# Kernel tuning notes

Hardware: AMD Instinct MI355X
Metric: run time of the kernel (lower is better)

The kernel has to match this reference:

```python
import jax, jax.numpy as jnp
import numpy as np

B, H, V = 64, 512, 20000
Lc, Lce, Lkb, R, E, T = 128, 64, 256, 32, 128, 32
SOS = 2
NEG = -1e9


def setup_inputs() -> dict:
    key = jax.random.key(0)
    ks = jax.random.split(key, 24)
    f = lambda i, shape, s: (jax.random.normal(ks[i], shape) * s).astype(jnp.float32)
    return dict(
        context_hidden=f(0, (1, B, H), 1.0),
        context_outputs=f(1, (B, Lc, H), 1.0),
        context_entity=f(2, (B, Lce, H), 1.0),
        kb_entity=f(3, (B, Lkb, H), 1.0),
        embed=f(4, (V, H), 0.1),
        Wp=f(5, (H, H), 0.05), bp=jnp.zeros((H,), jnp.float32),
        Wih=f(6, (3 * H, H), 0.05), Whh=f(7, (3 * H, H), 0.05),
        bih=jnp.zeros((3 * H,), jnp.float32), bhh=jnp.zeros((3 * H,), jnp.float32),
        Wg_ce=f(8, (H, H), 0.05), Wg_kb=f(9, (H, H), 0.05),
        Wq=f(10, (H, H), 0.05), Wm=f(11, (H, H), 0.05),
        v_attn=f(12, (H,), 0.05), b_attn=jnp.zeros((H,), jnp.float32),
        Wsw=f(13, (1, H), 0.05), bsw=jnp.zeros((1,), jnp.float32),
        Wc=f(14, (H, 3 * H), 0.05), bc=jnp.zeros((H,), jnp.float32),
        Wv=f(15, (V, H), 0.05), bv=jnp.zeros((V,), jnp.float32),
        context_entity_id=jax.random.randint(ks[16], (B, Lce), 0, E),
        kb_entity_id=jax.random.randint(ks[17], (B, Lkb), 0, E),
        kb_entity_row=jax.random.randint(ks[18], (B, Lkb), 0, R),
        context_mask=jnp.zeros((B, Lc), bool),
        context_entity_mask=jnp.zeros((B, Lce), bool),
        kb_entity_mask=jnp.zeros((B, Lkb), bool),
        target=jax.random.randint(ks[19], (B, T), 0, V),
    )


def gru_cell(x, h, Wih, Whh, bih, bhh):
    gi = x @ Wih.T + bih
    gh = h @ Whh.T + bhh
    ir, iz, inn = jnp.split(gi, 3, axis=-1)
    hr, hz, hn = jnp.split(gh, 3, axis=-1)
    r = jax.nn.sigmoid(ir + hr)
    z = jax.nn.sigmoid(iz + hz)
    n = jnp.tanh(inn + r * hn)
    return (1.0 - z) * n + z * h


def reference(context_hidden, context_outputs, context_entity, kb_entity,
              embed, Wp, bp, Wih, Whh, bih, bhh, Wg_ce, Wg_kb, Wq, Wm,
              v_attn, b_attn, Wsw, bsw, Wc, bc, Wv, bv,
              context_entity_id, kb_entity_id, kb_entity_row,
              context_mask, context_entity_mask, kb_entity_mask, target):
    B_, T_ = target.shape
    rows = jnp.arange(B_)[:, None]
    # dec_hidden = relu(projector(context_hidden))
    h0 = jax.nn.relu(context_hidden[0] @ Wp.T + bp)  # [B,H]
    # teacher forcing: input at step t is SOS for t=0, else target[:, t-1]
    dec_inputs = jnp.concatenate(
        [jnp.full((B_, 1), SOS, target.dtype), target[:, :-1]], axis=1)  # [B,T]

    # time-invariant KB row aggregation (to_onehot + bmm)
    onehot = jax.nn.one_hot(kb_entity_row, R, dtype=jnp.float32)
    onehot = onehot * (~kb_entity_mask)[..., None].astype(jnp.float32)  # [B,Lkb,R]
    row_onehot = jnp.swapaxes(onehot, 1, 2)  # [B,R,Lkb]
    row_hidden = jnp.einsum('brk,bkh->brh', row_onehot, kb_entity)  # [B,R,H]
    row_cnt = row_onehot.sum(2, keepdims=True)  # [B,R,1]
    row_empty = row_cnt[..., 0] == 0  # [B,R]
    row_hidden = row_hidden / jnp.clip(row_cnt, 1.0, None)
    # time-invariant mlp-attention memory projection
    mem_proj = jnp.einsum('bkh,gh->bkg', context_outputs, Wm)  # [B,Lc,H]

    def step(h, inp_t):
        x = embed[inp_t]  # [B,H] (dropout=0.0)
        h = gru_cell(x, h, Wih, Whh, bih, bhh)
        q = h
        # context-entity attention (general)
        qe = q @ Wg_ce.T
        logit_ce = jnp.einsum('bh,bkh->bk', qe, context_entity)
        logit_ce = jnp.where(context_entity_mask, NEG, logit_ce)
        w_ce = jax.nn.softmax(logit_ce, axis=1)
        ce_hidden = jnp.einsum('bk,bkh->bh', w_ce, context_entity)
        p_ctx = jnp.zeros((B_, E), jnp.float32).at[rows, context_entity_id].add(w_ce)
        # kb row-level attention (general)
        qk = q @ Wg_kb.T
        logit_row = jnp.einsum('bh,brh->br', qk, row_hidden)
        logit_row = jnp.where(row_empty, NEG, logit_row)
        w_row = jax.nn.softmax(logit_row, axis=1)
        kb_hidden = jnp.einsum('br,brh->bh', w_row, row_hidden)
        kb_row_pro = jnp.einsum('br,brk->bk', w_row, row_onehot)  # [B,Lkb]
        # within-row kb distribution: broadcast logits masked by row one-hot
        logit_kb = jnp.einsum('bh,bkh->bk', qk, kb_entity)[:, None, :]  # [B,1,Lkb]
        logit_kb = jnp.where(row_onehot > 0, logit_kb, NEG)  # [B,R,Lkb]
        pro_in_row = jax.nn.softmax(logit_kb, axis=2)
        pro_pos = jnp.take_along_axis(pro_in_row, kb_entity_row[:, None, :], axis=1)[:, 0, :]
        kb_pro = pro_pos * kb_row_pro  # [B,Lkb]
        p_kb = jnp.zeros((B_, E), jnp.float32).at[rows, kb_entity_id].add(kb_pro)
        # switch gate
        psw = jax.nn.sigmoid(q @ Wsw.T + bsw)  # [B,1]
        p_entity = (1.0 - psw) * p_ctx + psw * p_kb
        # mlp attention over context outputs
        logit_c = jnp.einsum('h,bkh->bk', v_attn,
                             jnp.tanh((q @ Wq.T)[:, None, :] + mem_proj + b_attn))
        logit_c = jnp.where(context_mask, NEG, logit_c)
        w_c = jax.nn.softmax(logit_c, axis=1)
        vocab_attn = jnp.einsum('bk,bkh->bh', w_c, context_outputs)
        entity_hidden = ce_hidden * (1.0 - psw) + kb_hidden * psw
        concat_out = jnp.tanh(
            jnp.concatenate([q, vocab_attn, entity_hidden], axis=1) @ Wc.T + bc)
        p_vocab = concat_out @ Wv.T + bv
        return h, (p_vocab, p_entity)

    _, (vocab_out, ptr_out) = jax.lax.scan(step, h0, dec_inputs.T)
    return vocab_out, ptr_out  # [T,B,V], [T,B,E]
```

## Files before the change

kernel.cpp:

```cpp
#include <hip/hip_runtime.h>
#include <math.h>


#define BN   64
#define HN   512
#define VN   20000
#define LCN  128
#define LCEN 64
#define LKBN 256
#define RN   32
#define EN   128
#define TN   32
#define NEGV -1e9f

typedef __attribute__((ext_vector_type(8))) short bf16x8;
typedef __attribute__((ext_vector_type(4))) float f32x4;

__device__ __forceinline__ float fast_tanh(float x) {
  float ax = fabsf(x);
  float e = __expf(-2.f * ax);
  float r = __fdividef(1.f - e, 1.f + e);
  return copysignf(r, x);
}
__device__ __forceinline__ float fast_sigm(float x) {
  return __fdividef(1.f, 1.f + __expf(-x));
}

__device__ __forceinline__ unsigned short f2bf(float f) {
  unsigned int u = __float_as_uint(f);
  unsigned int r = (u + 0x7FFFu + ((u >> 16) & 1u)) >> 16;
  return (unsigned short)r;
}

__device__ __forceinline__ void split8(const float* v, bf16x8& hi, bf16x8& lo) {
#pragma unroll
  for (int i = 0; i < 8; ++i) {
    unsigned short h = f2bf(v[i]);
    hi[i] = (short)h;
    lo[i] = (short)f2bf(v[i] - __uint_as_float((unsigned int)h << 16));
  }
}

template <int ACT, int TRS>
__global__ __launch_bounds__(256) void gemm_tile64(
    const float* __restrict__ A, const float* __restrict__ W,
    const float* __restrict__ bias, float* __restrict__ C,
    int M, int N, int K)
{
  __shared__ float As[16][68];
  __shared__ float Ws[16][68];
  int tid = threadIdx.x;
  int m0 = blockIdx.x * 64, n0 = blockIdx.y * 64;
  int lr = tid >> 2;
  int lk = (tid & 3) << 2;
  int ty = tid >> 4, tx = tid & 15;
  float acc[4][4] = {};
  const float* Ap = A + (size_t)(m0 + lr) * K + lk;
  const float* Wp = W + (size_t)(n0 + lr) * K + lk;
  bool aok = (m0 + lr) < M;
  bool wok = (n0 + lr) < N;
  for (int k0 = 0; k0 < K; k0 += 16) {
    float4 av = aok ? *(const float4*)(Ap + k0) : make_float4(0.f, 0.f, 0.f, 0.f);
    float4 wv = wok ? *(const float4*)(Wp + k0) : make_float4(0.f, 0.f, 0.f, 0.f);
    As[lk + 0][lr] = av.x; As[lk + 1][lr] = av.y; As[lk + 2][lr] = av.z; As[lk + 3][lr] = av.w;
    Ws[lk + 0][lr] = wv.x; Ws[lk + 1][lr] = wv.y; Ws[lk + 2][lr] = wv.z; Ws[lk + 3][lr] = wv.w;
    __syncthreads();
#pragma unroll
    for (int kk = 0; kk < 16; ++kk) {
      float4 a = *(const float4*)&As[kk][ty << 2];
      float4 w = *(const float4*)&Ws[kk][tx << 2];
      float ar[4] = {a.x, a.y, a.z, a.w};
      float wr[4] = {w.x, w.y, w.z, w.w};
#pragma unroll
      for (int i = 0; i < 4; ++i)
#pragma unroll
        for (int j = 0; j < 4; ++j) acc[i][j] += ar[i] * wr[j];
    }
    __syncthreads();
  }
#pragma unroll
  for (int i = 0; i < 4; ++i) {
    int m = m0 + (ty << 2) + i;
    if (m >= M) continue;
#pragma unroll
    for (int j = 0; j < 4; ++j) {
      int n = n0 + (tx << 2) + j;
      if (n >= N) continue;
      float v = acc[i][j] + (bias ? bias[n] : 0.f);
      if (ACT == 1) v = fmaxf(v, 0.f);
      if (TRS)
        C[((size_t)(m >> 7) * N + n) * 128 + (m & 127)] = v;
      else
        C[(size_t)m * N + n] = v;
    }
  }
}

template <int EPI, bool GATHER, bool PROJ>
__global__ __launch_bounds__(256) void gemm_mfma(
    const float* __restrict__ A, const float* __restrict__ W, int wstride,
    const float* __restrict__ bias, const int* __restrict__ target,
    const float* __restrict__ addm, int astride,
    const float* __restrict__ Wce, const float* __restrict__ Wkb,
    const float* __restrict__ Wq, const float* __restrict__ Wc,
    float* __restrict__ Cf, unsigned short* __restrict__ Cb,
    int M, int N, int K)
{
  int tid = threadIdx.x, wv = tid >> 6, lane = tid & 63;
  int m0 = blockIdx.x * 64, n0 = blockIdx.y * 64;
  int wm = (wv >> 1) * 32, wn = (wv & 1) * 32;
  int lr = lane & 15, kg = (lane >> 4) * 8;

  const float* arow[2];
#pragma unroll
  for (int mt = 0; mt < 2; ++mt) {
    int m = m0 + wm + mt * 16 + lr;
    if (GATHER) {
      int tt = m >> 6, bb = m & 63;
      int tok = (tt == 0) ? 2 : target[bb * TN + (tt - 1)];
      arow[mt] = A + (size_t)tok * K + kg;
    } else {
      arow[mt] = A + (size_t)m * K + kg;
    }
  }
  const float* wrow[2];
#pragma unroll
  for (int nt = 0; nt < 2; ++nt) {
    int nr = n0 + wn + nt * 16 + lr;
    if (PROJ) {
      if (nr < 512)       wrow[nt] = Wce + (size_t)nr * 512 + kg;
      else if (nr < 1024) wrow[nt] = Wkb + (size_t)(nr - 512) * 512 + kg;
      else if (nr < 1536) wrow[nt] = Wq + (size_t)(nr - 1024) * 512 + kg;
      else                wrow[nt] = Wc + (size_t)(nr - 1536) * 1536 + kg;
    } else {
      wrow[nt] = W + (size_t)nr * wstride + kg;
    }
  }

  f32x4 acc[2][2];
#pragma unroll
  for (int i = 0; i < 2; ++i)
#pragma unroll
    for (int j = 0; j < 2; ++j) acc[i][j] = (f32x4){0.f, 0.f, 0.f, 0.f};

  for (int ko = 0; ko < K; ko += 32) {
    bf16x8 ah[2], al[2], bh[2], bl[2];
#pragma unroll
    for (int mt = 0; mt < 2; ++mt) {
      float av[8];
      *(float4*)(av + 0) = *(const float4*)(arow[mt] + ko);
      *(float4*)(av + 4) = *(const float4*)(arow[mt] + ko + 4);
      split8(av, ah[mt], al[mt]);
    }
#pragma unroll
    for (int nt = 0; nt < 2; ++nt) {
      float wv8[8];
      *(float4*)(wv8 + 0) = *(const float4*)(wrow[nt] + ko);
      *(float4*)(wv8 + 4) = *(const float4*)(wrow[nt] + ko + 4);
      split8(wv8, bh[nt], bl[nt]);
    }
#pragma unroll
    for (int mt = 0; mt < 2; ++mt)
#pragma unroll
      for (int nt = 0; nt < 2; ++nt) {
        acc[mt][nt] = __builtin_amdgcn_mfma_f32_16x16x32_bf16(ah[mt], bh[nt], acc[mt][nt], 0, 0, 0);
        acc[mt][nt] = __builtin_amdgcn_mfma_f32_16x16x32_bf16(ah[mt], bl[nt], acc[mt][nt], 0, 0, 0);
        acc[mt][nt] = __builtin_amdgcn_mfma_f32_16x16x32_bf16(al[mt], bh[nt], acc[mt][nt], 0, 0, 0);
      }
  }

#pragma unroll
  for (int mt = 0; mt < 2; ++mt)
#pragma unroll
    for (int nt = 0; nt < 2; ++nt) {
      int col = n0 + wn + nt * 16 + lr;
      int rowb = m0 + wm + mt * 16 + (lane >> 4) * 4;
#pragma unroll
      for (int r = 0; r < 4; ++r) {
        int m = rowb + r;
        float v = acc[mt][nt][r];
        if (EPI == 0) {
          if (bias) v += bias[col];
          Cf[(size_t)m * N + col] = v;
        } else if (EPI == 2) {
          v += addm[(size_t)m * astride + col] + bias[col];
          Cb[(size_t)m * N + col] = f2bf(fast_tanh(v));
        } else {
          Cf[((size_t)(m >> 7) * N + col) * 128 + (m & 127)] = v;
        }
      }
    }
}

__global__ __launch_bounds__(256) void conv_bf16(
    const float* __restrict__ in, unsigned short* __restrict__ out, int n)
{
  int i = (blockIdx.x * 256 + threadIdx.x) * 4;
  if (i >= n) return;
  float4 v = *(const float4*)(in + i);
  out[i + 0] = f2bf(v.x);
  out[i + 1] = f2bf(v.y);
  out[i + 2] = f2bf(v.z);
  out[i + 3] = f2bf(v.w);
}

__global__ __launch_bounds__(256) void split_bf16k(
    const float* __restrict__ in, unsigned short* __restrict__ hi,
    unsigned short* __restrict__ lo, int n)
{
  int i = (blockIdx.x * 256 + threadIdx.x) * 4;
  if (i >= n) return;
  float4 v = *(const float4*)(in + i);
  float vv[4] = {v.x, v.y, v.z, v.w};
#pragma unroll
  for (int j = 0; j < 4; ++j) {
    unsigned short h = f2bf(vv[j]);
    hi[i + j] = h;
    lo[i + j] = f2bf(vv[j] - __uint_as_float((unsigned int)h << 16));
  }
}

__global__ __launch_bounds__(256) void row_agg(
    const float* __restrict__ kb, const int* __restrict__ krow,
    float* __restrict__ rowh, float* __restrict__ rowc)
{
  int b = blockIdx.x, tid = threadIdx.x;
  __shared__ float acc[RN * 256];
  __shared__ int rows[256];
  __shared__ float cnt_s[RN];
  rows[tid] = krow[b * LKBN + tid];
  __syncthreads();
  if (tid < RN) {
    int c = 0;
    for (int k = 0; k < LKBN; ++k) c += (rows[k] == tid);
    cnt_s[tid] = (float)c;
    rowc[b * RN + tid] = (float)c;
  }
  __syncthreads();
  for (int half = 0; half < 2; ++half) {
    int h = (half << 8) + tid;
    for (int r = 0; r < RN; ++r) acc[r * 256 + tid] = 0.f;
    for (int k = 0; k < LKBN; ++k)
      acc[rows[k] * 256 + tid] += kb[((size_t)b * LKBN + k) * HN + h];
    for (int r = 0; r < RN; ++r)
      rowh[((size_t)b * RN + r) * HN + h] = acc[r * 256 + tid] / fmaxf(cnt_s[r], 1.f);
  }
}

__global__ __launch_bounds__(256) void build_csr(
    const int* __restrict__ kbid, const int* __restrict__ ceid,
    const int* __restrict__ krow,
    int* __restrict__ kbo, int* __restrict__ kbi,
    int* __restrict__ ceo, int* __restrict__ cei,
    int* __restrict__ rwo, int* __restrict__ rwi)
{
  int b = blockIdx.x, tid = threadIdx.x;
  __shared__ int sid[256], srw[256], scid[64];
  __shared__ int cnt[128], off[129];
  sid[tid] = kbid[b * LKBN + tid];
  srw[tid] = krow[b * LKBN + tid];
  if (tid < 64) scid[tid] = ceid[b * LCEN + tid];
  __syncthreads();
  if (tid < 128) {
    int c = 0;
    for (int k = 0; k < 256; ++k) c += (sid[k] == tid);
    cnt[tid] = c;
  }
  __syncthreads();
  if (tid == 0) {
    int o = 0;
    for (int e = 0; e < 128; ++e) { off[e] = o; o += cnt[e]; }
    off[128] = o;
  }
  __syncthreads();
  if (tid < 128) {
    int w = off[tid];
    for (int k = 0; k < 256; ++k) if (sid[k] == tid) kbi[b * 256 + (w++)] = k;
    kbo[b * 129 + tid] = off[tid];
    if (tid == 0) kbo[b * 129 + 128] = off[128];
  }
  __syncthreads();
  if (tid < 128) {
    int c = 0;
    for (int k = 0; k < 64; ++k) c += (scid[k] == tid);
    cnt[tid] = c;
  }
  __syncthreads();
  if (tid == 0) {
    int o = 0;
    for (int e = 0; e < 128; ++e) { off[e] = o; o += cnt[e]; }
    off[128] = o;
  }
  __syncthreads();
  if (tid < 128) {
    int w = off[tid];
    for (int k = 0; k < 64; ++k) if (scid[k] == tid) cei[b * 64 + (w++)] = k;
    ceo[b * 129 + tid] = off[tid];
    if (tid == 0) ceo[b * 129 + 128] = off[128];
  }
  __syncthreads();
  if (tid < 32) {
    int c = 0;
    for (int k = 0; k < 256; ++k) c += (srw[k] == tid);
    cnt[tid] = c;
  }
  __syncthreads();
  if (tid == 0) {
    int o = 0;
    for (int r = 0; r < 32; ++r) { off[r] = o; o += cnt[r]; }
    off[32] = o;
  }
  __syncthreads();
  if (tid < 32) {
    int w = off[tid];
    for (int k = 0; k < 256; ++k) if (srw[k] == tid) rwi[b * 256 + (w++)] = k;
    rwo[b * 33 + tid] = off[tid];
    if (tid == 0) rwo[b * 33 + 32] = off[32];
  }
}

__global__ __launch_bounds__(256) void step_gru(
    const float* __restrict__ Gx, const float* __restrict__ hprev,
    float* __restrict__ hnew, const unsigned short* __restrict__ WhhH,
    const unsigned short* __restrict__ WhhL, const float* __restrict__ bhh)
{
  int tid = threadIdx.x;
  int wv = tid >> 6, lane = tid & 63;
  int j0 = blockIdx.x * 16;
  int m0 = wv * 16;
  int lr = lane & 15, kg = (lane >> 4) * 8;
  f32x4 acc[3];
#pragma unroll
  for (int g = 0; g < 3; ++g) acc[g] = (f32x4){0.f, 0.f, 0.f, 0.f};
  const float* ap = hprev + (size_t)(m0 + lr) * 512 + kg;
  const unsigned short* bhp = WhhH + (size_t)(j0 + lr) * 512 + kg;
  const unsigned short* blp = WhhL + (size_t)(j0 + lr) * 512 + kg;
#pragma unroll 4
  for (int ks = 0; ks < 16; ++ks) {
    int ko = ks * 32;
    float av[8];
    *(float4*)(av + 0) = *(const float4*)(ap + ko);
    *(float4*)(av + 4) = *(const float4*)(ap + ko + 4);
    bf16x8 ah, al;
    split8(av, ah, al);
#pragma unroll
    for (int g = 0; g < 3; ++g) {
      bf16x8 bh = *(const bf16x8*)(bhp + (size_t)g * 512 * 512 + ko);
      bf16x8 bl = *(const bf16x8*)(blp + (size_t)g * 512 * 512 + ko);
      acc[g] = __builtin_amdgcn_mfma_f32_16x16x32_bf16(ah, bh, acc[g], 0, 0, 0);
      acc[g] = __builtin_amdgcn_mfma_f32_16x16x32_bf16(ah, bl, acc[g], 0, 0, 0);
      acc[g] = __builtin_amdgcn_mfma_f32_16x16x32_bf16(al, bh, acc[g], 0, 0, 0);
    }
  }
  int j = j0 + lr;
#pragma unroll
  for (int r = 0; r < 4; ++r) {
    int b = m0 + (lane >> 4) * 4 + r;
    const float* gx = Gx + (size_t)b * 1536;
    float rr = fast_sigm(gx[j] + acc[0][r] + bhh[j]);
    float z  = fast_sigm(gx[512 + j] + acc[1][r] + bhh[512 + j]);
    float n  = fast_tanh(gx[1024 + j] + rr * (acc[2][r] + bhh[1024 + j]));
    float hp = hprev[(size_t)b * 512 + j];
    hnew[(size_t)b * 512 + j] = (1.f - z) * n + z * hp;
  }
}

__global__ __launch_bounds__(256) void attn_qk(
    const float* __restrict__ qp, const float* __restrict__ kb,
    const float* __restrict__ ce, const float* __restrict__ rowh,
    float* __restrict__ logits)
{
  int b = blockIdx.x, nt = blockIdx.y;
  int tid = threadIdx.x, wv = tid >> 6, lane = tid & 63;
  int lr = lane & 15, kg = (lane >> 4) * 8;
  const float* keys; int keybase, qoff, gkbase;
  if (nt < 8)       { keys = kb + (size_t)b * 256 * 512;  keybase = nt * 32;       qoff = 512; gkbase = keybase; }
  else if (nt < 10) { keys = ce + (size_t)b * 64 * 512;   keybase = (nt - 8) * 32; qoff = 0;   gkbase = 256 + keybase; }
  else              { keys = rowh + (size_t)b * 32 * 512; keybase = 0;             qoff = 512; gkbase = 320; }
  int mhalf = wv >> 1, nhalf = wv & 1;
  const float* ap = qp + (size_t)((mhalf * 16 + lr) * 64 + b) * 2048 + qoff + kg;
  const float* bp = keys + (size_t)(keybase + nhalf * 16 + lr) * 512 + kg;
  f32x4 acc = {0.f, 0.f, 0.f, 0.f};
#pragma unroll 4
  for (int ks = 0; ks < 16; ++ks) {
    int ko = ks * 32;
    float av[8], bv[8];
    *(float4*)(av + 0) = *(const float4*)(ap + ko);
    *(float4*)(av + 4) = *(const float4*)(ap + ko + 4);
    *(float4*)(bv + 0) = *(const float4*)(bp + ko);
    *(float4*)(bv + 4) = *(const float4*)(bp + ko + 4);
    bf16x8 ah, al, bh, bl;
    split8(av, ah, al);
    split8(bv, bh, bl);
    acc = __builtin_amdgcn_mfma_f32_16x16x32_bf16(ah, bh, acc, 0, 0, 0);
    acc = __builtin_amdgcn_mfma_f32_16x16x32_bf16(ah, bl, acc, 0, 0, 0);
    acc = __builtin_amdgcn_mfma_f32_16x16x32_bf16(al, bh, acc, 0, 0, 0);
  }
  int gk = gkbase + nhalf * 16 + lr;
#pragma unroll
  for (int r = 0; r < 4; ++r) {
    int t = mhalf * 16 + (lane >> 4) * 4 + r;
    logits[((size_t)b * 32 + t) * 352 + gk] = acc[r];
  }
}

__global__ __launch_bounds__(256) void attn_mlp(
    const float* __restrict__ qp, const float* __restrict__ mempT,
    const float* __restrict__ va, const float* __restrict__ ba,
    float* __restrict__ pmlp)
{
  int b = blockIdx.x, ch = blockIdx.y, tg = blockIdx.z;
  int tid = threadIdx.x;
  int h0 = ch << 7;
  __shared__ float sq[8][128];
  __shared__ float sv[128];
  for (int idx = tid; idx < 1024; idx += 256) {
    int tl = idx >> 7, i = idx & 127;
    int t = tg * 8 + tl;
    sq[tl][i] = qp[(size_t)(t * 64 + b) * 2048 + 1024 + h0 + i] + ba[h0 + i];
  }
  if (tid < 128) sv[tid] = va[h0 + tid];
  __syncthreads();
  int k = tid & 127, th = tid >> 7;
  const float* mp = mempT + ((size_t)b * 512 + h0) * 128 + k;
  float acc[4] = {};
  for (int h = 0; h < 128; ++h) {
    float mv = mp[h * 128];
    float vah = sv[h];
#pragma unroll
    for (int i = 0; i < 4; ++i)
      acc[i] += vah * fast_tanh(sq[th * 4 + i][h] + mv);
  }
#pragma unroll
  for (int i = 0; i < 4; ++i) {
    int t = tg * 8 + th * 4 + i;
    pmlp[(((size_t)b * 4 + ch) * 32 + t) * 128 + k] = acc[i];
  }
}

__global__ __launch_bounds__(256) void attn_reduce_all(
    const float* __restrict__ logits, const float* __restrict__ pmlp,
    const float* __restrict__ hall, const float* __restrict__ Wsw,
    const float* __restrict__ bsw, const int* __restrict__ krow,
    const int* __restrict__ kbo, const int* __restrict__ kbi,
    const int* __restrict__ ceo, const int* __restrict__ cei,
    const int* __restrict__ rwo, const int* __restrict__ rwi,
    float* __restrict__ pout, float* __restrict__ wall,
    float* __restrict__ pswall)
{
  int b = blockIdx.x, t = blockIdx.y, tid = threadIdx.x;
  int wv = tid >> 6, lane = tid & 63;
  __shared__ float s_l[480];
  __shared__ float s_kbp[256];
  __shared__ float s_wce[64], s_wrow[32], s_wc[128];
  __shared__ float s_rmax[32], s_rsum[32];
  __shared__ int s_krow[256];
  __shared__ float s_red[4];
  __shared__ float s_psw;

  const float* lg = logits + ((size_t)b * 32 + t) * 352;
  for (int k = tid; k < 352; k += 256) s_l[k] = lg[k];
  if (tid < 128) {
    const float* pm = pmlp + ((size_t)b * 4 * 32 + t) * 128 + tid;
    s_l[352 + tid] = pm[0] + pm[4096] + pm[8192] + pm[12288];
  }
  {
    const float* hp = hall + ((size_t)(t + 1) * 64 + b) * 512;
    float ps = hp[tid] * Wsw[tid] + hp[tid + 256] * Wsw[tid + 256];
    for (int o = 32; o; o >>= 1) ps += __shfl_down(ps, o);
    if (lane == 0) s_red[wv] = ps;
  }
  s_krow[tid] = krow[b * LKBN + tid];
  __syncthreads();
  if (tid == 0) s_psw = fast_sigm(s_red[0] + s_red[1] + s_red[2] + s_red[3] + bsw[0]);

  if (wv == 0) {
    {
      float v = s_l[256 + lane];
      float m = v;
      for (int o = 32; o; o >>= 1) m = fmaxf(m, __shfl_xor(m, o));
      float e = __expf(v - m), s = e;
      for (int o = 32; o; o >>= 1) s += __shfl_xor(s, o);
      s_wce[lane] = e / s;
    }
    {
      float v;
      if (lane < 32) {
        bool empty = rwo[b * 33 + lane + 1] == rwo[b * 33 + lane];
        v = empty ? NEGV : s_l[320 + lane];
      } else v = -INFINITY;
      float m = v;
      for (int o = 32; o; o >>= 1) m = fmaxf(m, __shfl_xor(m, o));
      float e = (lane < 32) ? __expf(v - m) : 0.f, s = e;
      for (int o = 32; o; o >>= 1) s += __shfl_xor(s, o);
      if (lane < 32) s_wrow[lane] = e / s;
    }
  } else if (wv == 1) {
    float v0 = s_l[352 + lane], v1 = s_l[352 + 64 + lane];
    float m = fmaxf(v0, v1);
    for (int o = 32; o; o >>= 1) m = fmaxf(m, __shfl_xor(m, o));
    float e0 = __expf(v0 - m), e1 = __expf(v1 - m);
    float s = e0 + e1;
    for (int o = 32; o; o >>= 1) s += __shfl_xor(s, o);
    s_wc[lane] = e0 / s;
    s_wc[lane + 64] = e1 / s;
  } else {
    int r = (tid - 128) >> 2, i = (tid - 128) & 3;
    int p0 = rwo[b * 33 + r], p1 = rwo[b * 33 + r + 1];
    float m = -INFINITY;
    for (int p = p0 + i; p < p1; p += 4) m = fmaxf(m, s_l[rwi[b * 256 + p]]);
    for (int o = 2; o; o >>= 1) m = fmaxf(m, __shfl_xor(m, o));
    float s = 0.f;
    for (int p = p0 + i; p < p1; p += 4) s += __expf(s_l[rwi[b * 256 + p]] - m);
    for (int o = 2; o; o >>= 1) s += __shfl_xor(s, o);
    if (i == 0) { s_rmax[r] = m; s_rsum[r] = s; }
  }
  __syncthreads();
  {
    int r = s_krow[tid];
    s_kbp[tid] = __expf(s_l[tid] - s_rmax[r]) / s_rsum[r] * s_wrow[r];
  }
  __syncthreads();
  if (tid < EN) {
    float a = 0.f;
    for (int p = ceo[b * 129 + tid]; p < ceo[b * 129 + tid + 1]; ++p)
      a += s_wce[cei[b * 64 + p]];
    float pk = 0.f;
    for (int p = kbo[b * 129 + tid]; p < kbo[b * 129 + tid + 1]; ++p)
      pk += s_kbp[kbi[b * 256 + p]];
    float psw = s_psw;
    pout[((size_t)t * BN + b) * EN + tid] = (1.f - psw) * a + psw * pk;
  }
  float* wb = wall + (size_t)(b * 32 + t) * 224;
  if (tid < 64) wb[tid] = s_wce[tid];
  else if (tid < 96) wb[tid] = s_wrow[tid - 64];
  else if (tid < 224) wb[tid] = s_wc[tid - 96];
  if (tid == 0) pswall[b * 32 + t] = s_psw;
}

__global__ __launch_bounds__(256) void attn_wsum_all(
    const float* __restrict__ wall, const float* __restrict__ pswall,
    const float* __restrict__ ctx, const float* __restrict__ ce,
    const float* __restrict__ rowh, float* __restrict__ cinall)
{
  int b = blockIdx.x, half = blockIdx.y, kind = blockIdx.z;
  int tid = threadIdx.x;
  int h = half * 256 + tid;
  if (kind == 0) {
    __shared__ float wc[32][128];
    for (int idx = tid; idx < 4096; idx += 256)
      wc[idx >> 7][idx & 127] = wall[(size_t)(b * 32 + (idx >> 7)) * 224 + 96 + (idx & 127)];
    __syncthreads();
    const float* xb = ctx + (size_t)b * 128 * 512 + h;
    float acc[32] = {};
    for (int k = 0; k < 128; k += 4) {
      float v0 = xb[(k + 0) * 512], v1 = xb[(k + 1) * 512];
      float v2 = xb[(k + 2) * 512], v3 = xb[(k + 3) * 512];
#pragma unroll
      for (int t = 0; t < 32; ++t) {
        float4 w = *(const float4*)&wc[t][k];
        acc[t] += w.x * v0 + w.y * v1 + w.z * v2 + w.w * v3;
      }
    }
    for (int t = 0; t < 32; ++t)
      cinall[(size_t)(t * 64 + b) * 1024 + h] = acc[t];
  } else {
    __shared__ float wce[32][64];
    __shared__ float wr[32][32];
    __shared__ float sps[32];
    for (int idx = tid; idx < 2048; idx += 256)
      wce[idx >> 6][idx & 63] = wall[(size_t)(b * 32 + (idx >> 6)) * 224 + (idx & 63)];
    for (int idx = tid; idx < 1024; idx += 256)
      wr[idx >> 5][idx & 31] = wall[(size_t)(b * 32 + (idx >> 5)) * 224 + 64 + (idx & 31)];
    if (tid < 32) sps[tid] = pswall[b * 32 + tid];
    __syncthreads();
    const float* cb = ce + (size_t)b * 64 * 512 + h;
    float ac[32] = {};
    for (int k = 0; k < 64; k += 4) {
      float v0 = cb[(k + 0) * 512], v1 = cb[(k + 1) * 512];
      float v2 = cb[(k + 2) * 512], v3 = cb[(k + 3) * 512];
#pragma unroll
      for (int t = 0; t < 32; ++t) {
        float4 w = *(const float4*)&wce[t][k];
        ac[t] += w.x * v0 + w.y * v1 + w.z * v2 + w.w * v3;
      }
    }
    const float* rb = rowh + (size_t)b * 32 * 512 + h;
    float ar[32] = {};
    for (int k = 0; k < 32; k += 4) {
      float v0 = rb[(k + 0) * 512], v1 = rb[(k + 1) * 512];
      float v2 = rb[(k + 2) * 512], v3 = rb[(k + 3) * 512];
#pragma unroll
      for (int t = 0; t < 32; ++t) {
        float4 w = *(const float4*)&wr[t][k];
        ar[t] += w.x * v0 + w.y * v1 + w.z * v2 + w.w * v3;
      }
    }
    for (int t = 0; t < 32; ++t) {
      float p = sps[t];
      cinall[(size_t)(t * 64 + b) * 1024 + 512 + h] = ac[t] * (1.f - p) + ar[t] * p;
    }
  }
}

__global__ __launch_bounds__(256) void gemm_vocab(
    const unsigned short* __restrict__ Ab, const unsigned short* __restrict__ Wb,
    const float* __restrict__ bv, float* __restrict__ C)
{
  int lid = blockIdx.x;
  int c = lid & 7, q = lid >> 3, i = q & 15, prow = q >> 4;
  int p = prow * 8 + c;
  if (p >= 157) return;
  int m0 = i * 128, n0 = p * 128;

  __shared__ __align__(16) unsigned short As[128 * 64];
  __shared__ __align__(16) unsigned short Bs[128 * 64];
  int tid = threadIdx.x;
  int wv = tid >> 6, lane = tid & 63;
  int wm = wv >> 1, wn = wv & 1;
  int srow = tid >> 3;
  int scb = (tid & 7) * 16;
  f32x4 acc[4][4];
#pragma unroll
  for (int a = 0; a < 4; ++a)
#pragma unroll
    for (int j = 0; j < 4; ++j) acc[a][j] = (f32x4){0.f, 0.f, 0.f, 0.f};

  for (int k0 = 0; k0 < 512; k0 += 64) {
    __syncthreads();
#pragma unroll
    for (int j = 0; j < 4; ++j) {
      int row = j * 32 + srow;
      uint4 va = *(const uint4*)(Ab + (size_t)(m0 + row) * 512 + k0 + (tid & 7) * 8);
      int brow = n0 + row;
      if (brow > VN - 1) brow = VN - 1;
      uint4 vb = *(const uint4*)(Wb + (size_t)brow * 512 + k0 + (tid & 7) * 8);
      int off = row * 128 + (scb ^ ((row & 7) << 4));
      *(uint4*)((char*)As + off) = va;
      *(uint4*)((char*)Bs + off) = vb;
    }
    __syncthreads();
#pragma unroll
    for (int ks = 0; ks < 2; ++ks) {
      bf16x8 af[4], bf[4];
#pragma unroll
      for (int m = 0; m < 4; ++m) {
        int r = wm * 64 + m * 16 + (lane & 15);
        int cb = (ks * 64 + (lane >> 4) * 16) ^ ((r & 7) << 4);
        af[m] = *(const bf16x8*)((const char*)As + r * 128 + cb);
      }
#pragma unroll
      for (int n = 0; n < 4; ++n) {
        int r = wn * 64 + n * 16 + (lane & 15);
        int cb = (ks * 64 + (lane >> 4) * 16) ^ ((r & 7) << 4);
        bf[n] = *(const bf16x8*)((const char*)Bs + r * 128 + cb);
      }
#pragma unroll
      for (int m = 0; m < 4; ++m)
#pragma unroll
        for (int n = 0; n < 4; ++n)
          acc[m][n] = __builtin_amdgcn_mfma_f32_16x16x32_bf16(af[m], bf[n], acc[m][n], 0, 0, 0);
    }
  }
#pragma unroll
  for (int n = 0; n < 4; ++n) {
    int col = n0 + wn * 64 + n * 16 + (lane & 15);
    if (col >= VN) continue;
    float bvv = bv[col];
#pragma unroll
    for (int m = 0; m < 4; ++m) {
      int rowb = m0 + wm * 64 + m * 16 + (lane >> 4) * 4;
#pragma unroll
      for (int r = 0; r < 4; ++r)
        C[(size_t)(rowb + r) * VN + col] = acc[m][n][r] + bvv;
    }
  }
}

extern "C" void kernel_launch(void* const* d_in, const int* in_sizes, int n_in,
                              void* d_out, int out_size, void* d_ws, size_t ws_size,
                              hipStream_t stream)
{
  const float* ch   = (const float*)d_in[0];
  const float* ctx  = (const float*)d_in[1];
  const float* ce   = (const float*)d_in[2];
  const float* kb   = (const float*)d_in[3];
  const float* emb  = (const float*)d_in[4];
  const float* Wp   = (const float*)d_in[5];
  const float* bp   = (const float*)d_in[6];
  const float* Wih  = (const float*)d_in[7];
  const float* Whh  = (const float*)d_in[8];
  const float* bih  = (const float*)d_in[9];
  const float* bhh  = (const float*)d_in[10];
  const float* Wgce = (const float*)d_in[11];
  const float* Wgkb = (const float*)d_in[12];
  const float* Wq   = (const float*)d_in[13];
  const float* Wm   = (const float*)d_in[14];
  const float* va   = (const float*)d_in[15];
  const float* ba   = (const float*)d_in[16];
  const float* Wsw  = (const float*)d_in[17];
  const float* bsw  = (const float*)d_in[18];
  const float* Wc   = (const float*)d_in[19];
  const float* bc   = (const float*)d_in[20];
  const float* Wv   = (const float*)d_in[21];
  const float* bv   = (const float*)d_in[22];
  const int* ce_id  = (const int*)d_in[23];
  const int* kb_id  = (const int*)d_in[24];
  const int* kb_row = (const int*)d_in[25];
  const int* target = (const int*)d_in[29];

  float* ws = (float*)d_ws;
  float* rowh   = ws;
  float* rowc   = rowh + 1048576;
  float* mempT  = rowc + 2048;
  float* hall   = mempT + 4194304;
  float* Gx     = hall + 1081344;
  float* qp     = Gx + 3145728;
  float* logits = qp + 4194304;
  float* pmlp   = logits + 720896;
  float* wall   = pmlp + 1048576;
  float* pswall = wall + 458752;
  float* cinall = pswall + 2048;
  unsigned short* callb = (unsigned short*)(cinall + 2097152);
  unsigned short* Wvb   = (unsigned short*)(cinall + 2097152 + 524288);
  unsigned short* WhhH  = (unsigned short*)(cinall + 2097152 + 524288 + 5120000);
  unsigned short* WhhL  = (unsigned short*)(cinall + 2097152 + 524288 + 5120000 + 393216);
  int* kbo = (int*)(cinall + 2097152 + 524288 + 5120000 + 786432);
  int* kbi = kbo + 64 * 129;
  int* ceo = kbi + 64 * 256;
  int* cei = ceo + 64 * 129;
  int* rwo = cei + 64 * 64;
  int* rwi = rwo + 64 * 33;

  float* vout = (float*)d_out;
  float* pout = vout + (size_t)TN * BN * VN;

  row_agg<<<BN, 256, 0, stream>>>(kb, kb_row, rowh, rowc);
  conv_bf16<<<10000, 256, 0, stream>>>(Wv, Wvb, VN * HN);
  split_bf16k<<<768, 256, 0, stream>>>(Whh, WhhH, WhhL, 1536 * 512);
  build_csr<<<BN, 256, 0, stream>>>(kb_id, ce_id, kb_row, kbo, kbi, ceo, cei,
                                    rwo, rwi);
  gemm_tile64<1, 0><<<dim3(1, 8), 256, 0, stream>>>(ch, Wp, bp, hall, BN, HN, HN);
  gemm_mfma<3, false, false><<<dim3(128, 8), 256, 0, stream>>>(
      ctx, Wm, 512, nullptr, nullptr, nullptr, 0,
      nullptr, nullptr, nullptr, nullptr, mempT, nullptr, 8192, 512, 512);
  gemm_mfma<0, true, false><<<dim3(32, 24), 256, 0, stream>>>(
      emb, Wih, 512, bih, target, nullptr, 0,
      nullptr, nullptr, nullptr, nullptr, Gx, nullptr, 2048, 1536, 512);

  for (int t = 0; t < TN; ++t)
    step_gru<<<32, 256, 0, stream>>>(
        Gx + (size_t)t * BN * 1536, hall + (size_t)t * BN * HN,
        hall + (size_t)(t + 1) * BN * HN, WhhH, WhhL, bhh);

  gemm_mfma<0, false, true><<<dim3(32, 32), 256, 0, stream>>>(
      hall + BN * HN, nullptr, 0, nullptr, nullptr, nullptr, 0,
      Wgce, Wgkb, Wq, Wc, qp, nullptr, 2048, 2048, 512);
  attn_qk<<<dim3(BN, 11), 256, 0, stream>>>(qp, kb, ce, rowh, logits);
  attn_mlp<<<dim3(BN, 4, 4), 256, 0, stream>>>(qp, mempT, va, ba, pmlp);
  attn_reduce_all<<<dim3(BN, TN), 256, 0, stream>>>(
      logits, pmlp, hall, Wsw, bsw, kb_row, kbo, kbi, ceo, cei, rwo, rwi,
      pout, wall, pswall);
  attn_wsum_all<<<dim3(BN, 2, 2), 256, 0, stream>>>(wall, pswall, ctx, ce,
                                                    rowh, cinall);
  gemm_mfma<2, false, false><<<dim3(32, 8), 256, 0, stream>>>(
      cinall, Wc + 512, 1536, bc, nullptr, qp + 1536, 2048,
      nullptr, nullptr, nullptr, nullptr, nullptr, callb, 2048, 512, 1024);
  gemm_vocab<<<2560, 256, 0, stream>>>(callb, Wvb, bv, vout);
}
```

Baseline: 1.168 ms.

## Persistent GRU kernel with grid barrier and merge setup/attention launches

Replaces the 32 per-timestep GRU launches with one persistent 32-block kernel that loops over timesteps and synchronises blocks through an atomic counter barrier in global memory. It also merges the two weight-conversion kernels, the row-aggregation and CSR-building kernels, and the two attention kernels into single launches to cut launch count. The spin barrier relies on all 32 blocks being co-resident. It adds a memset and fence/atomic latency per step.

```diff
diff --git a/kernel.cpp b/kernel.cpp
--- a/kernel.cpp
+++ b/kernel.cpp
@@ -192,44 +192,54 @@
     }
 }
 
-__global__ __launch_bounds__(256) void conv_bf16(
-    const float* __restrict__ in, unsigned short* __restrict__ out, int n)
-{
-  int i = (blockIdx.x * 256 + threadIdx.x) * 4;
-  if (i >= n) return;
-  float4 v = *(const float4*)(in + i);
-  out[i + 0] = f2bf(v.x);
-  out[i + 1] = f2bf(v.y);
-  out[i + 2] = f2bf(v.z);
-  out[i + 3] = f2bf(v.w);
-}
-
-__global__ __launch_bounds__(256) void split_bf16k(
-    const float* __restrict__ in, unsigned short* __restrict__ hi,
-    unsigned short* __restrict__ lo, int n)
-{
-  int i = (blockIdx.x * 256 + threadIdx.x) * 4;
-  if (i >= n) return;
-  float4 v = *(const float4*)(in + i);
-  float vv[4] = {v.x, v.y, v.z, v.w};
-#pragma unroll
-  for (int j = 0; j < 4; ++j) {
-    unsigned short h = f2bf(vv[j]);
-    hi[i + j] = h;
-    lo[i + j] = f2bf(vv[j] - __uint_as_float((unsigned int)h << 16));
-  }
-}
-
-__global__ __launch_bounds__(256) void row_agg(
+__global__ __launch_bounds__(256) void conv_split(
+    const float* __restrict__ Wv, unsigned short* __restrict__ Wvb,
+    const float* __restrict__ Whh, unsigned short* __restrict__ WhhH,
+    unsigned short* __restrict__ WhhL)
+{
+  int bid = blockIdx.x;
+  if (bid < 10000) {
+    int i = (bid * 256 + threadIdx.x) * 4;
+    if (i >= VN * HN) return;
+    float4 v = *(const float4*)(Wv + i);
+    Wvb[i + 0] = f2bf(v.x);
+    Wvb[i + 1] = f2bf(v.y);
+    Wvb[i + 2] = f2bf(v.z);
+    Wvb[i + 3] = f2bf(v.w);
+  } else {
+    int i = ((bid - 10000) * 256 + threadIdx.x) * 4;
+    if (i >= 1536 * 512) return;
+    float4 v = *(const float4*)(Whh + i);
+    float vv[4] = {v.x, v.y, v.z, v.w};
+#pragma unroll
+    for (int j = 0; j < 4; ++j) {
+      unsigned short h = f2bf(vv[j]);
+      WhhH[i + j] = h;
+      WhhL[i + j] = f2bf(vv[j] - __uint_as_float((unsigned int)h << 16));
+    }
+  }
+}
+
+__global__ __launch_bounds__(256) void setup_b(
     const float* __restrict__ kb, const int* __restrict__ krow,
-    float* __restrict__ rowh, float* __restrict__ rowc)
+    const int* __restrict__ kbid, const int* __restrict__ ceid,
+    float* __restrict__ rowh, float* __restrict__ rowc,
+    int* __restrict__ kbo, int* __restrict__ kbi,
+    int* __restrict__ ceo, int* __restrict__ cei,
+    int* __restrict__ rwo, int* __restrict__ rwi)
 {
   int b = blockIdx.x, tid = threadIdx.x;
   __shared__ float acc[RN * 256];
   __shared__ int rows[256];
   __shared__ float cnt_s[RN];
+  __shared__ int sid[256], scid[64];
+  __shared__ int cnt[128], off[129];
+
   rows[tid] = krow[b * LKBN + tid];
-  __syncthreads();
+  sid[tid] = kbid[b * LKBN + tid];
+  if (tid < 64) scid[tid] = ceid[b * LCEN + tid];
+  __syncthreads();
+
   if (tid < RN) {
     int c = 0;
     for (int k = 0; k < LKBN; ++k) c += (rows[k] == tid);
@@ -245,22 +255,8 @@
     for (int r = 0; r < RN; ++r)
       rowh[((size_t)b * RN + r) * HN + h] = acc[r * 256 + tid] / fmaxf(cnt_s[r], 1.f);
   }
-}
-
-__global__ __launch_bounds__(256) void build_csr(
-    const int* __restrict__ kbid, const int* __restrict__ ceid,
-    const int* __restrict__ krow,
-    int* __restrict__ kbo, int* __restrict__ kbi,
-    int* __restrict__ ceo, int* __restrict__ cei,
-    int* __restrict__ rwo, int* __restrict__ rwi)
-{
-  int b = blockIdx.x, tid = threadIdx.x;
-  __shared__ int sid[256], srw[256], scid[64];
-  __shared__ int cnt[128], off[129];
-  sid[tid] = kbid[b * LKBN + tid];
-  srw[tid] = krow[b * LKBN + tid];
-  if (tid < 64) scid[tid] = ceid[b * LCEN + tid];
-  __syncthreads();
+  __syncthreads();
+
   if (tid < 128) {
     int c = 0;
     for (int k = 0; k < 256; ++k) c += (sid[k] == tid);
@@ -301,7 +297,7 @@
   __syncthreads();
   if (tid < 32) {
     int c = 0;
-    for (int k = 0; k < 256; ++k) c += (srw[k] == tid);
+    for (int k = 0; k < 256; ++k) c += (rows[k] == tid);
     cnt[tid] = c;
   }
   __syncthreads();
@@ -313,128 +309,147 @@
   __syncthreads();
   if (tid < 32) {
     int w = off[tid];
-    for (int k = 0; k < 256; ++k) if (srw[k] == tid) rwi[b * 256 + (w++)] = k;
+    for (int k = 0; k < 256; ++k) if (rows[k] == tid) rwi[b * 256 + (w++)] = k;
     rwo[b * 33 + tid] = off[tid];
     if (tid == 0) rwo[b * 33 + 32] = off[32];
   }
 }
 
-__global__ __launch_bounds__(256) void step_gru(
-    const float* __restrict__ Gx, const float* __restrict__ hprev,
-    float* __restrict__ hnew, const unsigned short* __restrict__ WhhH,
-    const unsigned short* __restrict__ WhhL, const float* __restrict__ bhh)
+__global__ __launch_bounds__(256) void gru_chain(
+    const float* __restrict__ Gx0, float* __restrict__ hall,
+    const unsigned short* __restrict__ WhhH,
+    const unsigned short* __restrict__ WhhL,
+    const float* __restrict__ bhh, int* __restrict__ bar)
 {
   int tid = threadIdx.x;
   int wv = tid >> 6, lane = tid & 63;
   int j0 = blockIdx.x * 16;
   int m0 = wv * 16;
   int lr = lane & 15, kg = (lane >> 4) * 8;
-  f32x4 acc[3];
-#pragma unroll
-  for (int g = 0; g < 3; ++g) acc[g] = (f32x4){0.f, 0.f, 0.f, 0.f};
-  const float* ap = hprev + (size_t)(m0 + lr) * 512 + kg;
+  int j = j0 + lr;
   const unsigned short* bhp = WhhH + (size_t)(j0 + lr) * 512 + kg;
   const unsigned short* blp = WhhL + (size_t)(j0 + lr) * 512 + kg;
+
+  for (int t = 0; t < TN; ++t) {
+    const float* Gx = Gx0 + (size_t)t * BN * 1536;
+    const float* hprev = hall + (size_t)t * BN * HN;
+    float* hnew = hall + (size_t)(t + 1) * BN * HN;
+
+    f32x4 acc[3];
+#pragma unroll
+    for (int g = 0; g < 3; ++g) acc[g] = (f32x4){0.f, 0.f, 0.f, 0.f};
+    const float* ap = hprev + (size_t)(m0 + lr) * 512 + kg;
 #pragma unroll 4
-  for (int ks = 0; ks < 16; ++ks) {
-    int ko = ks * 32;
-    float av[8];
-    *(float4*)(av + 0) = *(const float4*)(ap + ko);
-    *(float4*)(av + 4) = *(const float4*)(ap + ko + 4);
-    bf16x8 ah, al;
-    split8(av, ah, al);
-#pragma unroll
-    for (int g = 0; g < 3; ++g) {
-      bf16x8 bh = *(const bf16x8*)(bhp + (size_t)g * 512 * 512 + ko);
-      bf16x8 bl = *(const bf16x8*)(blp + (size_t)g * 512 * 512 + ko);
-      acc[g] = __builtin_amdgcn_mfma_f32_16x16x32_bf16(ah, bh, acc[g], 0, 0, 0);
-      acc[g] = __builtin_amdgcn_mfma_f32_16x16x32_bf16(ah, bl, acc[g], 0, 0, 0);
-      acc[g] = __builtin_amdgcn_mfma_f32_16x16x32_bf16(al, bh, acc[g], 0, 0, 0);
-    }
-  }
-  int j = j0 + lr;
-#pragma unroll
-  for (int r = 0; r < 4; ++r) {
-    int b = m0 + (lane >> 4) * 4 + r;
-    const float* gx = Gx + (size_t)b * 1536;
-    float rr = fast_sigm(gx[j] + acc[0][r] + bhh[j]);
-    float z  = fast_sigm(gx[512 + j] + acc[1][r] + bhh[512 + j]);
-    float n  = fast_tanh(gx[1024 + j] + rr * (acc[2][r] + bhh[1024 + j]));
-    float hp = hprev[(size_t)b * 512 + j];
-    hnew[(size_t)b * 512 + j] = (1.f - z) * n + z * hp;
-  }
-}
-
-__global__ __launch_bounds__(256) void attn_qk(
+    for (int ks = 0; ks < 16; ++ks) {
+      int ko = ks * 32;
+      float av[8];
+      *(float4*)(av + 0) = *(const float4*)(ap + ko);
+      *(float4*)(av + 4) = *(const float4*)(ap + ko + 4);
+      bf16x8 ah, al;
+      split8(av, ah, al);
+#pragma unroll
+      for (int g = 0; g < 3; ++g) {
+        bf16x8 bh = *(const bf16x8*)(bhp + (size_t)g * 512 * 512 + ko);
+        bf16x8 bl = *(const bf16x8*)(blp + (size_t)g * 512 * 512 + ko);
+        acc[g] = __builtin_amdgcn_mfma_f32_16x16x32_bf16(ah, bh, acc[g], 0, 0, 0);
+        acc[g] = __builtin_amdgcn_mfma_f32_16x16x32_bf16(ah, bl, acc[g], 0, 0, 0);
+        acc[g] = __builtin_amdgcn_mfma_f32_16x16x32_bf16(al, bh, acc[g], 0, 0, 0);
+      }
+    }
+#pragma unroll
+    for (int r = 0; r < 4; ++r) {
+      int b = m0 + (lane >> 4) * 4 + r;
+      const float* gx = Gx + (size_t)b * 1536;
+      float rr = fast_sigm(gx[j] + acc[0][r] + bhh[j]);
+      float z  = fast_sigm(gx[512 + j] + acc[1][r] + bhh[512 + j]);
+      float n  = fast_tanh(gx[1024 + j] + rr * (acc[2][r] + bhh[1024 + j]));
+      float hp = hprev[(size_t)b * 512 + j];
+      hnew[(size_t)b * 512 + j] = (1.f - z) * n + z * hp;
+    }
+
+    if (t < TN - 1) {
+      __syncthreads();
+      if (tid == 0) {
+        __threadfence();
+        atomicAdd(bar, 1);
+        int target = 32 * (t + 1);
+        while (atomicAdd(bar, 0) < target) __builtin_amdgcn_s_sleep(2);
+      }
+      __syncthreads();
+      __threadfence();
+    }
+  }
+}
+
+__global__ __launch_bounds__(256) void attn_logits(
     const float* __restrict__ qp, const float* __restrict__ kb,
     const float* __restrict__ ce, const float* __restrict__ rowh,
-    float* __restrict__ logits)
+    const float* __restrict__ mempT, const float* __restrict__ va,
+    const float* __restrict__ ba, float* __restrict__ logits,
+    float* __restrict__ pmlp)
 {
   int b = blockIdx.x, nt = blockIdx.y;
-  int tid = threadIdx.x, wv = tid >> 6, lane = tid & 63;
-  int lr = lane & 15, kg = (lane >> 4) * 8;
-  const float* keys; int keybase, qoff, gkbase;
-  if (nt < 8)       { keys = kb + (size_t)b * 256 * 512;  keybase = nt * 32;       qoff = 512; gkbase = keybase; }
-  else if (nt < 10) { keys = ce + (size_t)b * 64 * 512;   keybase = (nt - 8) * 32; qoff = 0;   gkbase = 256 + keybase; }
-  else              { keys = rowh + (size_t)b * 32 * 512; keybase = 0;             qoff = 512; gkbase = 320; }
-  int mhalf = wv >> 1, nhalf = wv & 1;
-  const float* ap = qp + (size_t)((mhalf * 16 + lr) * 64 + b) * 2048 + qoff + kg;
-  const float* bp = keys + (size_t)(keybase + nhalf * 16 + lr) * 512 + kg;
-  f32x4 acc = {0.f, 0.f, 0.f, 0.f};
+  int tid = threadIdx.x;
+  if (nt < 11) {
+    int wv = tid >> 6, lane = tid & 63;
+    int lr = lane & 15, kg = (lane >> 4) * 8;
+    const float* keys; int keybase, qoff, gkbase;
+    if (nt < 8)       { keys = kb + (size_t)b * 256 * 512;  keybase = nt * 32;       qoff = 512; gkbase = keybase; }
+    else if (nt < 10) { keys = ce + (size_t)b * 64 * 512;   keybase = (nt - 8) * 32; qoff = 0;   gkbase = 256 + keybase; }
+    else              { keys = rowh + (size_t)b * 32 * 512; keybase = 0;             qoff = 512; gkbase = 320; }
+    int mhalf = wv >> 1, nhalf = wv & 1;
+    const float* ap = qp + (size_t)((mhalf * 16 + lr) * 64 + b) * 2048 + qoff + kg;
+    const float* bp = keys + (size_t)(keybase + nhalf * 16 + lr) * 512 + kg;
+    f32x4 acc = {0.f, 0.f, 0.f, 0.f};
 #pragma unroll 4
-  for (int ks = 0; ks < 16; ++ks) {
-    int ko = ks * 32;
-    float av[8], bv[8];
-    *(float4*)(av + 0) = *(const float4*)(ap + ko);
-    *(float4*)(av + 4) = *(const float4*)(ap + ko + 4);
-    *(float4*)(bv + 0) = *(const float4*)(bp + ko);
-    *(float4*)(bv + 4) = *(const float4*)(bp + ko + 4);
-    bf16x8 ah, al, bh, bl;
-    split8(av, ah, al);
-    split8(bv, bh, bl);
-    acc = __builtin_amdgcn_mfma_f32_16x16x32_bf16(ah, bh, acc, 0, 0, 0);
-    acc = __builtin_amdgcn_mfma_f32_16x16x32_bf16(ah, bl, acc, 0, 0, 0);
-    acc = __builtin_amdgcn_mfma_f32_16x16x32_bf16(al, bh, acc, 0, 0, 0);
-  }
-  int gk = gkbase + nhalf * 16 + lr;
-#pragma unroll
-  for (int r = 0; r < 4; ++r) {
-    int t = mhalf * 16 + (lane >> 4) * 4 + r;
-    logits[((size_t)b * 32 + t) * 352 + gk] = acc[r];
-  }
-}
-
-__global__ __launch_bounds__(256) void attn_mlp(
-    const float* __restrict__ qp, const float* __restrict__ mempT,
-    const float* __restrict__ va, const float* __restrict__ ba,
-    float* __restrict__ pmlp)
-{
-  int b = blockIdx.x, ch = blockIdx.y, tg = blockIdx.z;
-  int tid = threadIdx.x;
-  int h0 = ch << 7;
-  __shared__ float sq[8][128];
-  __shared__ float sv[128];
-  for (int idx = tid; idx < 1024; idx += 256) {
-    int tl = idx >> 7, i = idx & 127;
-    int t = tg * 8 + tl;
-    sq[tl][i] = qp[(size_t)(t * 64 + b) * 2048 + 1024 + h0 + i] + ba[h0 + i];
-  }
-  if (tid < 128) sv[tid] = va[h0 + tid];
-  __syncthreads();
-  int k = tid & 127, th = tid >> 7;
-  const float* mp = mempT + ((size_t)b * 512 + h0) * 128 + k;
-  float acc[4] = {};
-  for (int h = 0; h < 128; ++h) {
-    float mv = mp[h * 128];
-    float vah = sv[h];
-#pragma unroll
-    for (int i = 0; i < 4; ++i)
-      acc[i] += vah * fast_tanh(sq[th * 4 + i][h] + mv);
-  }
-#pragma unroll
-  for (int i = 0; i < 4; ++i) {
-    int t = tg * 8 + th * 4 + i;
-    pmlp[(((size_t)b * 4 + ch) * 32 + t) * 128 + k] = acc[i];
+    for (int ks = 0; ks < 16; ++ks) {
+      int ko = ks * 32;
+      float av[8], bv[8];
+      *(float4*)(av + 0) = *(const float4*)(ap + ko);
+      *(float4*)(av + 4) = *(const float4*)(ap + ko + 4);
+      *(float4*)(bv + 0) = *(const float4*)(bp + ko);
+      *(float4*)(bv + 4) = *(const float4*)(bp + ko + 4);
+      bf16x8 ah, al, bh, bl;
+      split8(av, ah, al);
+      split8(bv, bh, bl);
+      acc = __builtin_amdgcn_mfma_f32_16x16x32_bf16(ah, bh, acc, 0, 0, 0);
+      acc = __builtin_amdgcn_mfma_f32_16x16x32_bf16(ah, bl, acc, 0, 0, 0);
+      acc = __builtin_amdgcn_mfma_f32_16x16x32_bf16(al, bh, acc, 0, 0, 0);
+    }
+    int gk = gkbase + nhalf * 16 + lr;
+#pragma unroll
+    for (int r = 0; r < 4; ++r) {
+      int t = mhalf * 16 + (lane >> 4) * 4 + r;
+      logits[((size_t)b * 32 + t) * 352 + gk] = acc[r];
+    }
+  } else {
+    int zz = nt - 11;
+    int ch = zz & 3, tg = zz >> 2;
+    int h0 = ch << 7;
+    __shared__ float sq[8][128];
+    __shared__ float sv[128];
+    for (int idx = tid; idx < 1024; idx += 256) {
+      int tl = idx >> 7, i = idx & 127;
+      int t = tg * 8 + tl;
+      sq[tl][i] = qp[(size_t)(t * 64 + b) * 2048 + 1024 + h0 + i] + ba[h0 + i];
+    }
+    if (tid < 128) sv[tid] = va[h0 + tid];
+    __syncthreads();
+    int k = tid & 127, th = tid >> 7;
+    const float* mp = mempT + ((size_t)b * 512 + h0) * 128 + k;
+    float acc[4] = {};
+    for (int h = 0; h < 128; ++h) {
+      float mv = mp[h * 128];
+      float vah = sv[h];
+#pragma unroll
+      for (int i = 0; i < 4; ++i)
+        acc[i] += vah * fast_tanh(sq[th * 4 + i][h] + mv);
+    }
+#pragma unroll
+    for (int i = 0; i < 4; ++i) {
+      int t = tg * 8 + th * 4 + i;
+      pmlp[(((size_t)b * 4 + ch) * 32 + t) * 128 + k] = acc[i];
+    }
   }
 }
 
@@ -731,15 +746,15 @@
   int* cei = ceo + 64 * 129;
   int* rwo = cei + 64 * 64;
   int* rwi = rwo + 64 * 33;
+  int* bar = rwi + 64 * 256;
 
   float* vout = (float*)d_out;
   float* pout = vout + (size_t)TN * BN * VN;
 
-  row_agg<<<BN, 256, 0, stream>>>(kb, kb_row, rowh, rowc);
-  conv_bf16<<<10000, 256, 0, stream>>>(Wv, Wvb, VN * HN);
-  split_bf16k<<<768, 256, 0, stream>>>(Whh, WhhH, WhhL, 1536 * 512);
-  build_csr<<<BN, 256, 0, stream>>>(kb_id, ce_id, kb_row, kbo, kbi, ceo, cei,
-                                    rwo, rwi);
+  hipMemsetAsync(bar, 0, sizeof(int), stream);
+  setup_b<<<BN, 256, 0, stream>>>(kb, kb_row, kb_id, ce_id, rowh, rowc,
+                                  kbo, kbi, ceo, cei, rwo, rwi);
+  conv_split<<<10768, 256, 0, stream>>>(Wv, Wvb, Whh, WhhH, WhhL);
   gemm_tile64<1, 0><<<dim3(1, 8), 256, 0, stream>>>(ch, Wp, bp, hall, BN, HN, HN);
   gemm_mfma<3, false, false><<<dim3(128, 8), 256, 0, stream>>>(
       ctx, Wm, 512, nullptr, nullptr, nullptr, 0,
@@ -748,16 +763,13 @@
       emb, Wih, 512, bih, target, nullptr, 0,
       nullptr, nullptr, nullptr, nullptr, Gx, nullptr, 2048, 1536, 512);
 
-  for (int t = 0; t < TN; ++t)
-    step_gru<<<32, 256, 0, stream>>>(
-        Gx + (size_t)t * BN * 1536, hall + (size_t)t * BN * HN,
-        hall + (size_t)(t + 1) * BN * HN, WhhH, WhhL, bhh);
+  gru_chain<<<32, 256, 0, stream>>>(Gx, hall, WhhH, WhhL, bhh, bar);
 
   gemm_mfma<0, false, true><<<dim3(32, 32), 256, 0, stream>>>(
       hall + BN * HN, nullptr, 0, nullptr, nullptr, nullptr, 0,
       Wgce, Wgkb, Wq, Wc, qp, nullptr, 2048, 2048, 512);
-  attn_qk<<<dim3(BN, 11), 256, 0, stream>>>(qp, kb, ce, rowh, logits);
-  attn_mlp<<<dim3(BN, 4, 4), 256, 0, stream>>>(qp, mempT, va, ba, pmlp);
+  attn_logits<<<dim3(BN, 27), 256, 0, stream>>>(qp, kb, ce, rowh, mempT,
+                                                va, ba, logits, pmlp);
   attn_reduce_all<<<dim3(BN, TN), 256, 0, stream>>>(
       logits, pmlp, hall, Wsw, bsw, kb_row, kbo, kbi, ceo, cei, rwo, rwi,
       pout, wall, pswall);
```

Result: slower. 1.352 ms (+15.7%).
